# Kernel tuning notes

Measured on AMD Instinct MI355X. Metric: run time of the kernel, lower is better.

The kernel has to match this reference:

```python
import jax, jax.numpy as jnp
import numpy as np

# Typical Deformable-DETR pyramid for an 800x1200 image, strides 8/16/32/64
SPATIAL = np.array([[100, 150], [50, 75], [25, 38], [13, 19]], dtype=np.int64)


def setup_inputs() -> dict:
    key = jax.random.key(0)
    k1, k2, k3 = jax.random.split(key, 3)
    bs, heads, d, L, P = 2, 8, 32, 4, 4
    num_keys = int((SPATIAL[:, 0] * SPATIAL[:, 1]).sum())  # 18947
    Q = num_keys  # encoder self-attention: one query per key
    value = jax.random.normal(k1, (bs, num_keys, heads, d), dtype=jnp.float32)
    # normalized sampling coords in [0,1] (module maps to [-1,1] via 2*x-1)
    sampling_locations = jax.random.uniform(k2, (bs, Q, heads, L, P, 2), dtype=jnp.float32)
    w = jax.random.uniform(k3, (bs, Q, heads, L, P), dtype=jnp.float32)
    attention_weights = jax.nn.softmax(w.reshape(bs, Q, heads, L * P), axis=-1).reshape(bs, Q, heads, L, P)
    return {
        "value": value,
        "value_spatial_shapes": jnp.asarray(SPATIAL),
        "sampling_locations": sampling_locations,
        "attention_weights": attention_weights,
    }


def _bilinear_sample(v, grid):
    """F.grid_sample(mode='bilinear', padding_mode='zeros', align_corners=False).
    v: (N, H, W, d); grid: (N, Q, P, 2) with (x, y) in [-1, 1].
    Returns (N, Q, P, d)."""
    N, H, W, d = v.shape
    x = (grid[..., 0] + 1.0) * (W * 0.5) - 0.5
    y = (grid[..., 1] + 1.0) * (H * 0.5) - 0.5
    x0 = jnp.floor(x).astype(jnp.int32)
    y0 = jnp.floor(y).astype(jnp.int32)
    x1, y1 = x0 + 1, y0 + 1
    wx1 = x - x0
    wy1 = y - y0
    wx0 = 1.0 - wx1
    wy0 = 1.0 - wy1
    nidx = jnp.arange(N)[:, None, None]

    def gather(yy, xx):
        m = ((xx >= 0) & (xx < W) & (yy >= 0) & (yy < H)).astype(v.dtype)
        out = v[nidx, jnp.clip(yy, 0, H - 1), jnp.clip(xx, 0, W - 1)]  # (N,Q,P,d)
        return out * m[..., None]

    return (gather(y0, x0) * (wy0 * wx0)[..., None]
            + gather(y0, x1) * (wy0 * wx1)[..., None]
            + gather(y1, x0) * (wy1 * wx0)[..., None]
            + gather(y1, x1) * (wy1 * wx1)[..., None])


def reference(value, value_spatial_shapes, sampling_locations, attention_weights):
    shapes = np.asarray(value_spatial_shapes)  # static level shapes
    bs, num_keys, heads, d = value.shape
    _, Q, _, L, P, _ = sampling_locations.shape
    grids = 2.0 * sampling_locations - 1.0  # (bs,Q,heads,L,P,2)
    sampled = []
    start = 0
    for lvl in range(L):
        H, W = int(shapes[lvl, 0]), int(shapes[lvl, 1])
        v = value[:, start:start + H * W]  # (bs, H*W, heads, d)
        start += H * W
        v = v.transpose(0, 2, 1, 3).reshape(bs * heads, H, W, d)
        g = grids[:, :, :, lvl].transpose(0, 2, 1, 3, 4).reshape(bs * heads, Q, P, 2)
        sampled.append(_bilinear_sample(v, g))  # (bs*heads, Q, P, d)
    s = jnp.stack(sampled, axis=2)  # (bs*heads, Q, L, P, d)
    w = attention_weights.transpose(0, 2, 1, 3, 4).reshape(bs * heads, Q, L, P)
    out = jnp.einsum('nqlpd,nqlp->nqd', s, w)  # (bs*heads, Q, d)
    # feature layout matches torch: channel index = head*d + c
    return out.reshape(bs, heads, Q, d).transpose(0, 2, 1, 3).reshape(bs, Q, heads * d)
```

## Files before the change

kernel.cpp:

```cpp
#include <hip/hip_runtime.h>
#include <hip/hip_fp16.h>


#define KQ 19947
#define NBQ (2 * KQ)

__global__ __launch_bounds__(256) void transpose_f16(
    const float* __restrict__ V, __half* __restrict__ Vh)
{
    const int pair = blockIdx.y;
    const int j = blockIdx.x * 256 + threadIdx.x;
    if (j >= KQ * 4) return;
    const int k = j >> 2, cg = j & 3;
    const int b = pair >> 3, h = pair & 7;
    const float* src = V + (((size_t)b * KQ + k) * 8 + h) * 32 + cg * 8;
    const float4 a0 = *reinterpret_cast<const float4*>(src);
    const float4 a1 = *reinterpret_cast<const float4*>(src + 4);
    __half2 h0 = __floats2half2_rn(a0.x, a0.y);
    __half2 h1 = __floats2half2_rn(a0.z, a0.w);
    __half2 h2 = __floats2half2_rn(a1.x, a1.y);
    __half2 h3 = __floats2half2_rn(a1.z, a1.w);
    uint4 o;
    o.x = *reinterpret_cast<unsigned int*>(&h0);
    o.y = *reinterpret_cast<unsigned int*>(&h1);
    o.z = *reinterpret_cast<unsigned int*>(&h2);
    o.w = *reinterpret_cast<unsigned int*>(&h3);
    reinterpret_cast<uint4*>(Vh + ((size_t)pair * KQ) * 32)[j] = o;
}

template<int ROUND>
static __device__ __forceinline__ void shared_point(
    int j, float2 g, float w,
    int& offb0, int& offb1, float& dxx, float& wy0w, float& wy1w)
{
    const bool hi = (j & 4) != 0;
    const int Wl = (ROUND == 0) ? (hi ? 75 : 150) : (hi ? 19 : 38);
    const int Hl = (ROUND == 0) ? (hi ? 50 : 100) : (hi ? 13 : 25);
    const int st = (ROUND == 0) ? (hi ? 15000 : 0) : (hi ? 19700 : 18750);
    const float Wf = (float)Wl, Hf = (float)Hl;
    const float x = fmaf(g.x, Wf, -0.5f);
    const float y = fmaf(g.y, Hf, -0.5f);
    const float fy = floorf(y);
    const int y0 = (int)fy;
    const int x0 = (int)floorf(x);
    const int bx = min(max(x0, 0), Wl - 2);
    dxx = x - (float)bx;
    const float wy1 = y - fy, wy0 = 1.f - wy1;
    const int y0c = max(y0, 0);
    const int y1c = min(y0 + 1, Hl - 1);
    const float ay0 = (y0 >= 0) ? wy0 : 0.f;
    const float ay1 = (y0 + 1 < Hl) ? wy1 : 0.f;
    wy0w = w * ay0;
    wy1w = w * ay1;
    offb0 = (st + y0c * Wl + bx) << 5;
    offb1 = (st + y1c * Wl + bx) << 5;
}

static __device__ __forceinline__ void consume_level(
    const uint4* v, const float* cw, float acc[8])
{
    __half2 accH[4];
    #pragma unroll
    for (int j = 0; j < 4; ++j) accH[j] = __half2(__half(0.f), __half(0.f));
    #pragma unroll
    for (int i = 0; i < 8; ++i) {
        const __half2 wh = __floats2half2_rn(cw[i], cw[i]);
        union { uint4 u; __half2 h2[4]; } uv;
        uv.u = v[i];
        #pragma unroll
        for (int j = 0; j < 4; ++j)
            accH[j] = __hfma2(wh, uv.h2[j], accH[j]);
    }
    #pragma unroll
    for (int j = 0; j < 4; ++j) {
        const float2 f = __half22float2(accH[j]);
        acc[2*j]   += f.x;
        acc[2*j+1] += f.y;
    }
}

#define GLOAD8(buf, obase)                                                   \
    {                                                                        \
        _Pragma("unroll")                                                    \
        for (int i = 0; i < 8; ++i) {                                        \
            const __half* p_ = vbl + (obase)[i];                             \
            asm volatile("global_load_dwordx4 %0, %1, off"                   \
                         : "=v"(buf[i]) : "v"(p_));                          \
        }                                                                    \
    }
#define VWAIT(n)                                                             \
    asm volatile("s_waitcnt vmcnt(" #n ")" ::: "memory");                    \
    __builtin_amdgcn_sched_barrier(0)
#define SBAR() __builtin_amdgcn_sched_barrier(0)

__global__ __launch_bounds__(256, 3) void msda_fwd_t(
    const __half* __restrict__ Vh,
    const float* __restrict__ LOC,
    const float* __restrict__ W,
    float* __restrict__ OUT)
{
    const int pair = blockIdx.x & 15;
    const int qc   = blockIdx.x >> 4;
    const int tid  = threadIdx.x;
    const int s    = tid & 7;
    const int slot = s >> 2;
    const float slotf = (float)slot;
    const int q    = qc * 32 + (tid >> 3);
    if (q >= KQ) return;
    const int b = pair >> 3, h = pair & 7;
    const int ln = tid & 63;
    const int gb = ln & 56;

    const __half* vbl = Vh + (size_t)pair * KQ * 32 + s * 8;
    const float* lp = LOC + (((size_t)b * KQ + q) * 8 + h) * 32;
    const float* wp = W   + (((size_t)b * KQ + q) * 8 + h) * 16;

    float acc[8];
    #pragma unroll
    for (int c = 0; c < 8; ++c) acc[c] = 0.f;

    const float2 gA = *reinterpret_cast<const float2*>(lp + 2 * s);
    const float  wA = wp[s];
    const float2 gB = *reinterpret_cast<const float2*>(lp + 2 * s + 16);
    const float  wB = wp[s + 8];

    int ob0A, ob1A, ob0B, ob1B;
    float dxA, u0A, u1A, dxB, u0B, u1B;
    shared_point<0>(s, gA, wA, ob0A, ob1A, dxA, u0A, u1A);
    shared_point<1>(s, gB, wB, ob0B, ob1B, dxB, u0B, u1B);

    int off[32];
    float cw[32];
    #pragma unroll
    for (int pt = 0; pt < 8; ++pt) {
        const int src = gb + pt;
        const int   o0 = __shfl(ob0A, src, 64);
        const int   o1 = __shfl(ob1A, src, 64);
        const float dx = __shfl(dxA,  src, 64);
        const float u0 = __shfl(u0A,  src, 64);
        const float u1 = __shfl(u1A,  src, 64);
        const float wxl = fmaxf(0.f, 1.f - fabsf(dx - slotf));
        off[2*pt]   = o0;
        off[2*pt+1] = o1;
        cw[2*pt]    = u0 * wxl;
        cw[2*pt+1]  = u1 * wxl;
    }
    #pragma unroll
    for (int pt = 0; pt < 8; ++pt) {
        const int src = gb + pt;
        const int   o0 = __shfl(ob0B, src, 64);
        const int   o1 = __shfl(ob1B, src, 64);
        const float dx = __shfl(dxB,  src, 64);
        const float u0 = __shfl(u0B,  src, 64);
        const float u1 = __shfl(u1B,  src, 64);
        const float wxl = fmaxf(0.f, 1.f - fabsf(dx - slotf));
        off[16+2*pt]   = o0;
        off[16+2*pt+1] = o1;
        cw[16+2*pt]    = u0 * wxl;
        cw[16+2*pt+1]  = u1 * wxl;
    }

    VWAIT(0);

    uint4 va[8], vb2[8], vc[8];
    GLOAD8(va,  off + 0);
    GLOAD8(vb2, off + 8);
    VWAIT(8);
    GLOAD8(vc,  off + 16);
    SBAR();
    consume_level(va, cw + 0, acc);
    SBAR();
    GLOAD8(va,  off + 24);
    VWAIT(16);
    consume_level(vb2, cw + 8, acc);
    VWAIT(8);
    consume_level(vc, cw + 16, acc);
    VWAIT(0);
    consume_level(va, cw + 24, acc);

    #pragma unroll
    for (int c = 0; c < 8; ++c)
        acc[c] += __shfl_xor(acc[c], 4, 64);

    float* op = OUT + ((size_t)b * KQ + q) * 256 + h * 32 + (s & 3) * 8 + slot * 4;
    *reinterpret_cast<float4*>(op) =
        make_float4(acc[slot*4], acc[slot*4+1], acc[slot*4+2], acc[slot*4+3]);
}

static __device__ __forceinline__ void fmadd4(float4& a, float s, const float4 v) {
    a.x = fmaf(s, v.x, a.x);
    a.y = fmaf(s, v.y, a.y);
    a.z = fmaf(s, v.z, a.z);
    a.w = fmaf(s, v.w, a.w);
}

__global__ __launch_bounds__(256, 4) void msda_fwd_f32(
    const float* __restrict__ V,
    const float* __restrict__ LOC,
    const float* __restrict__ W,
    float* __restrict__ OUT)
{
    const int t  = blockIdx.x * 256 + threadIdx.x;
    const int cg = t & 7;
    const int h  = (t >> 3) & 7;
    const int bq = t >> 6;
    if (bq >= NBQ) return;
    const int b = (bq >= KQ) ? 1 : 0;

    const int Hs[4]  = {100, 50, 25, 13};
    const int Ws[4]  = {150, 75, 38, 19};
    const int STs[4] = {0, 15000, 18750, 19700};

    const int hoff = (h << 5) + (cg << 2);
    const float* vb = V + (size_t)b * KQ * 256 + hoff;
    const float* lp = LOC + ((size_t)bq * 8 + h) * 32;
    const float* wp = W   + ((size_t)bq * 8 + h) * 16;

    float4 acc = make_float4(0.f, 0.f, 0.f, 0.f);

    #pragma unroll
    for (int l = 0; l < 4; ++l) {
        const int Hh = Hs[l], Ww = Ws[l], st = STs[l];
        const float Hf = (float)Hh, Wf = (float)Ww;
        const float4 w4 = *reinterpret_cast<const float4*>(wp + l * 4);
        const float4 g0 = *reinterpret_cast<const float4*>(lp + l * 8);
        const float4 g1 = *reinterpret_cast<const float4*>(lp + l * 8 + 4);
        const float lx[4] = {g0.x, g0.z, g1.x, g1.z};
        const float ly[4] = {g0.y, g0.w, g1.y, g1.w};
        const float ww[4] = {w4.x, w4.y, w4.z, w4.w};
        #pragma unroll
        for (int p = 0; p < 4; ++p) {
            const float x = fmaf(lx[p], Wf, -0.5f);
            const float y = fmaf(ly[p], Hf, -0.5f);
            const float fx = floorf(x), fy = floorf(y);
            const int x0 = (int)fx, y0 = (int)fy;
            const float wx1 = x - fx, wy1 = y - fy;
            const float wx0 = 1.f - wx1, wy0 = 1.f - wy1;
            const int x0c = max(x0, 0),     x1c = min(x0 + 1, Ww - 1);
            const int y0c = max(y0, 0),     y1c = min(y0 + 1, Hh - 1);
            const float ax0 = (x0 >= 0)      ? wx0 : 0.f;
            const float ax1 = (x0 + 1 < Ww)  ? wx1 : 0.f;
            const float ay0 = (y0 >= 0)      ? wy0 : 0.f;
            const float ay1 = (y0 + 1 < Hh)  ? wy1 : 0.f;
            const float w = ww[p];
            const int b0 = st + y0c * Ww, b1 = st + y1c * Ww;
            fmadd4(acc, w*ay0*ax0, *reinterpret_cast<const float4*>(vb + ((b0+x0c) << 8)));
            fmadd4(acc, w*ay0*ax1, *reinterpret_cast<const float4*>(vb + ((b0+x1c) << 8)));
            fmadd4(acc, w*ay1*ax0, *reinterpret_cast<const float4*>(vb + ((b1+x0c) << 8)));
            fmadd4(acc, w*ay1*ax1, *reinterpret_cast<const float4*>(vb + ((b1+x1c) << 8)));
        }
    }
    *reinterpret_cast<float4*>(OUT + (size_t)bq * 256 + hoff) = acc;
}

extern "C" void kernel_launch(void* const* d_in, const int* in_sizes, int n_in,
                              void* d_out, int out_size, void* d_ws, size_t ws_size,
                              hipStream_t stream) {
    const float* V   = (const float*)d_in[0];
    const float* LOC = (const float*)d_in[2];
    const float* W   = (const float*)d_in[3];
    float* OUT = (float*)d_out;

    const size_t n_val = (size_t)2 * KQ * 256;
    const size_t need  = n_val * sizeof(__half) + 256;

    if (ws_size >= need) {
        __half* Vh = (__half*)d_ws;
        const int jtot = KQ * 4;
        dim3 tgrid((jtot + 255) / 256, 16);
        hipLaunchKernelGGL(transpose_f16, tgrid, dim3(256), 0, stream, V, Vh);

        const int qchunks = (KQ + 31) / 32;
        const int blocks  = qchunks * 16;
        hipLaunchKernelGGL(msda_fwd_t, dim3(blocks), dim3(256), 0, stream,
                           Vh, LOC, W, OUT);
    } else {
        const int total = NBQ * 64;
        hipLaunchKernelGGL(msda_fwd_f32, dim3((total + 255) / 256), dim3(256), 0, stream,
                           V, LOC, W, OUT);
    }
}
```

Before: 84.52 us.

## Store horizontally paired texels for the two finest levels to halve gather rows

Adds a transpose kernel that writes each value pixel twice for levels 0 and 1, so that pixel x and x+1 sit side by side in one 64-half record. The sampler's offsets now point into this duplicated layout, so each row's left and right neighbours come from one contiguous 128-byte span. The aim is better coalescing and fewer distinct cache lines per bilinear gather. In exchange the workspace grows and the preprocessing pass writes roughly twice the data for the large levels, and this path runs only when the workspace is big enough.

```diff
diff --git a/kernel.cpp b/kernel.cpp
--- a/kernel.cpp
+++ b/kernel.cpp
@@ -5,15 +5,9 @@
 #define KQ 19947
 #define NBQ (2 * KQ)
 
-__global__ __launch_bounds__(256) void transpose_f16(
-    const float* __restrict__ V, __half* __restrict__ Vh)
-{
-    const int pair = blockIdx.y;
-    const int j = blockIdx.x * 256 + threadIdx.x;
-    if (j >= KQ * 4) return;
-    const int k = j >> 2, cg = j & 3;
-    const int b = pair >> 3, h = pair & 7;
-    const float* src = V + (((size_t)b * KQ + k) * 8 + h) * 32 + cg * 8;
+#define PAIR_HALVES 1228704
+
+static __device__ __forceinline__ uint4 pack8(const float* __restrict__ src) {
     const float4 a0 = *reinterpret_cast<const float4*>(src);
     const float4 a1 = *reinterpret_cast<const float4*>(src + 4);
     __half2 h0 = __floats2half2_rn(a0.x, a0.y);
@@ -25,10 +19,51 @@
     o.y = *reinterpret_cast<unsigned int*>(&h1);
     o.z = *reinterpret_cast<unsigned int*>(&h2);
     o.w = *reinterpret_cast<unsigned int*>(&h3);
+    return o;
+}
+
+__global__ __launch_bounds__(256) void transpose_f16(
+    const float* __restrict__ V, __half* __restrict__ Vh)
+{
+    const int pair = blockIdx.y;
+    const int j = blockIdx.x * 256 + threadIdx.x;
+    if (j >= KQ * 4) return;
+    const int k = j >> 2, cg = j & 3;
+    const int b = pair >> 3, h = pair & 7;
+    const uint4 o = pack8(V + (((size_t)b * KQ + k) * 8 + h) * 32 + cg * 8);
     reinterpret_cast<uint4*>(Vh + ((size_t)pair * KQ) * 32)[j] = o;
 }
 
-template<int ROUND>
+__global__ __launch_bounds__(256) void transpose_dup(
+    const float* __restrict__ V, __half* __restrict__ Vh)
+{
+    const int pair = blockIdx.y;
+    const int j = blockIdx.x * 256 + threadIdx.x;
+    if (j >= KQ * 4) return;
+    const int k = j >> 2, cg = j & 3;
+    const int b = pair >> 3, h = pair & 7;
+    const uint4 o = pack8(V + (((size_t)b * KQ + k) * 8 + h) * 32 + cg * 8);
+    __half* base = Vh + (size_t)pair * PAIR_HALVES;
+    int dst0 = -1, dst1 = -1;
+    if (k < 15000) {
+        const int y = k / 150, x = k - y * 150;
+        if (x <= 148) dst0 = (y * 149 + x) * 64 + cg * 8;
+        if (x >= 1)   dst1 = (y * 149 + x - 1) * 64 + 32 + cg * 8;
+    } else if (k < 18750) {
+        const int kk = k - 15000;
+        const int y = kk / 75, x = kk - y * 75;
+        if (x <= 73) dst0 = 953600 + (y * 74 + x) * 64 + cg * 8;
+        if (x >= 1)  dst1 = 953600 + (y * 74 + x - 1) * 64 + 32 + cg * 8;
+    } else if (k < 19700) {
+        dst0 = 1190400 + (k - 18750) * 32 + cg * 8;
+    } else {
+        dst0 = 1220800 + (k - 19700) * 32 + cg * 8;
+    }
+    if (dst0 >= 0) *reinterpret_cast<uint4*>(base + dst0) = o;
+    if (dst1 >= 0) *reinterpret_cast<uint4*>(base + dst1) = o;
+}
+
+template<int ROUND, bool DUP>
 static __device__ __forceinline__ void shared_point(
     int j, float2 g, float w,
     int& offb0, int& offb1, float& dxx, float& wy0w, float& wy1w)
@@ -36,7 +71,6 @@
     const bool hi = (j & 4) != 0;
     const int Wl = (ROUND == 0) ? (hi ? 75 : 150) : (hi ? 19 : 38);
     const int Hl = (ROUND == 0) ? (hi ? 50 : 100) : (hi ? 13 : 25);
-    const int st = (ROUND == 0) ? (hi ? 15000 : 0) : (hi ? 19700 : 18750);
     const float Wf = (float)Wl, Hf = (float)Hl;
     const float x = fmaf(g.x, Wf, -0.5f);
     const float y = fmaf(g.y, Hf, -0.5f);
@@ -52,8 +86,22 @@
     const float ay1 = (y0 + 1 < Hl) ? wy1 : 0.f;
     wy0w = w * ay0;
     wy1w = w * ay1;
-    offb0 = (st + y0c * Wl + bx) << 5;
-    offb1 = (st + y1c * Wl + bx) << 5;
+    if (DUP) {
+        if (ROUND == 0) {
+            const int stride = Wl - 1;
+            const int baseH = hi ? 953600 : 0;
+            offb0 = baseH + ((y0c * stride + bx) << 6);
+            offb1 = baseH + ((y1c * stride + bx) << 6);
+        } else {
+            const int baseH = hi ? 1220800 : 1190400;
+            offb0 = baseH + ((y0c * Wl + bx) << 5);
+            offb1 = baseH + ((y1c * Wl + bx) << 5);
+        }
+    } else {
+        const int st = (ROUND == 0) ? (hi ? 15000 : 0) : (hi ? 19700 : 18750);
+        offb0 = (st + y0c * Wl + bx) << 5;
+        offb1 = (st + y1c * Wl + bx) << 5;
+    }
 }
 
 static __device__ __forceinline__ void consume_level(
@@ -93,6 +141,7 @@
     __builtin_amdgcn_sched_barrier(0)
 #define SBAR() __builtin_amdgcn_sched_barrier(0)
 
+template<bool DUP>
 __global__ __launch_bounds__(256, 3) void msda_fwd_t(
     const __half* __restrict__ Vh,
     const float* __restrict__ LOC,
@@ -111,7 +160,9 @@
     const int ln = tid & 63;
     const int gb = ln & 56;
 
-    const __half* vbl = Vh + (size_t)pair * KQ * 32 + s * 8;
+    const size_t pairBase = DUP ? ((size_t)pair * PAIR_HALVES)
+                                : ((size_t)pair * KQ * 32);
+    const __half* vbl = Vh + pairBase + s * 8;
     const float* lp = LOC + (((size_t)b * KQ + q) * 8 + h) * 32;
     const float* wp = W   + (((size_t)b * KQ + q) * 8 + h) * 16;
 
@@ -126,8 +177,8 @@
 
     int ob0A, ob1A, ob0B, ob1B;
     float dxA, u0A, u1A, dxB, u0B, u1B;
-    shared_point<0>(s, gA, wA, ob0A, ob1A, dxA, u0A, u1A);
-    shared_point<1>(s, gB, wB, ob0B, ob1B, dxB, u0B, u1B);
+    shared_point<0, DUP>(s, gA, wA, ob0A, ob1A, dxA, u0A, u1A);
+    shared_point<1, DUP>(s, gB, wB, ob0B, ob1B, dxB, u0B, u1B);
 
     int off[32];
     float cw[32];
@@ -261,18 +312,23 @@
     const float* W   = (const float*)d_in[3];
     float* OUT = (float*)d_out;
 
-    const size_t n_val = (size_t)2 * KQ * 256;
-    const size_t need  = n_val * sizeof(__half) + 256;
-
-    if (ws_size >= need) {
+    const size_t need_dup   = (size_t)16 * PAIR_HALVES * 2 + 256;
+    const size_t need_plain = (size_t)2 * KQ * 256 * 2 + 256;
+    const int jtot = KQ * 4;
+    const int qchunks = (KQ + 31) / 32;
+    const int gblocks = qchunks * 16;
+
+    if (ws_size >= need_dup) {
         __half* Vh = (__half*)d_ws;
-        const int jtot = KQ * 4;
+        dim3 tgrid((jtot + 255) / 256, 16);
+        hipLaunchKernelGGL(transpose_dup, tgrid, dim3(256), 0, stream, V, Vh);
+        hipLaunchKernelGGL((msda_fwd_t<true>), dim3(gblocks), dim3(256), 0, stream,
+                           Vh, LOC, W, OUT);
+    } else if (ws_size >= need_plain) {
+        __half* Vh = (__half*)d_ws;
         dim3 tgrid((jtot + 255) / 256, 16);
         hipLaunchKernelGGL(transpose_f16, tgrid, dim3(256), 0, stream, V, Vh);
-
-        const int qchunks = (KQ + 31) / 32;
-        const int blocks  = qchunks * 16;
-        hipLaunchKernelGGL(msda_fwd_t, dim3(blocks), dim3(256), 0, stream,
+        hipLaunchKernelGGL((msda_fwd_t<false>), dim3(gblocks), dim3(256), 0, stream,
                            Vh, LOC, W, OUT);
     } else {
         const int total = NBQ * 64;
```

Measured after the change: 106.5 us. +26.0%, slower.
